# Performance work log

Hardware: AMD Instinct MI355X
Metric: run time of the kernel (lower is better)

## Reference

```python
import jax, jax.numpy as jnp
import numpy as np

B, S, C = 64, 1024, 512
EPS = 1e-5

def setup_inputs() -> dict:
    key = jax.random.key(0)
    k1, k2, k3 = jax.random.split(key, 3)
    x = jax.random.normal(k1, (B, S, C), dtype=jnp.float32)
    # LayerNorm affine over normalized_shape=[S, C]
    ln_w = jnp.ones((S, C), dtype=jnp.float32)
    ln_b = jnp.zeros((S, C), dtype=jnp.float32)
    # Linear(seq_len, seq_len): torch init U(-1/sqrt(S), 1/sqrt(S))
    bound = 1.0 / np.sqrt(S)
    lin_w = jax.random.uniform(k2, (S, S), jnp.float32, -bound, bound)
    lin_b = jax.random.uniform(k3, (S,), jnp.float32, -bound, bound)
    return {"x": x, "ln_w": ln_w, "ln_b": ln_b, "lin_w": lin_w, "lin_b": lin_b}

def reference(x, ln_w, ln_b, lin_w, lin_b):
    # LayerNorm over last two dims [S, C]
    mu = jnp.mean(x, axis=(1, 2), keepdims=True)
    var = jnp.mean(jnp.square(x - mu), axis=(1, 2), keepdims=True)
    h = (x - mu) * jax.lax.rsqrt(var + EPS) * ln_w + ln_b
    # permute -> [B, C, S], linear over S, relu, permute back, residual
    # fused as einsum over the seq axis directly (no explicit transpose)
    y = jnp.einsum('bsc,ts->btc', h, lin_w) + lin_b[None, :, None]
    y = jax.nn.relu(y)
    return x + y
```

## Files before the change

kernel.cpp:

```cpp
#include <hip/hip_runtime.h>
#include <stdint.h>

#define BB 64
#define SS 1024
#define CC 512
#define EPS 1e-5f

typedef __attribute__((ext_vector_type(8))) __bf16 bf16x8;
typedef __attribute__((ext_vector_type(8))) unsigned short ushort8v;
typedef __attribute__((ext_vector_type(4))) float f32x4;

__device__ __forceinline__ unsigned short f2bf(float f) {
    unsigned int u = __builtin_bit_cast(unsigned int, f);
    u += 0x7fffu + ((u >> 16) & 1u);
    return (unsigned short)(u >> 16);
}

__global__ __launch_bounds__(256) void k_prep(const float* __restrict__ x,
                                              const float* __restrict__ w,
                                              float* __restrict__ psum,
                                              float* __restrict__ psq,
                                              unsigned short* __restrict__ wb) {
    int t = threadIdx.x;
    if (blockIdx.x >= 2048) {
        int i = (blockIdx.x - 2048) * 256 + t;
        float4 v = ((const float4*)w)[i];
        ushort4 o;
        o.x = f2bf(v.x); o.y = f2bf(v.y); o.z = f2bf(v.z); o.w = f2bf(v.w);
        ((ushort4*)wb)[i] = o;
        return;
    }
    int b = blockIdx.x >> 5, g = blockIdx.x & 31;
    const float4* x4 = (const float4*)(x + (size_t)b * SS * CC + (size_t)g * 16384);
    float s = 0.f, q = 0.f;
#pragma unroll
    for (int i = 0; i < 16; ++i) {
        float4 v = x4[t + i * 256];
        s += v.x + v.y + v.z + v.w;
        q += v.x * v.x + v.y * v.y + v.z * v.z + v.w * v.w;
    }
    for (int off = 32; off; off >>= 1) {
        s += __shfl_down(s, off, 64);
        q += __shfl_down(q, off, 64);
    }
    __shared__ float ls[4], lq[4];
    int wv = t >> 6;
    if ((t & 63) == 0) { ls[wv] = s; lq[wv] = q; }
    __syncthreads();
    if (t == 0) {
        psum[blockIdx.x] = ls[0] + ls[1] + ls[2] + ls[3];
        psq[blockIdx.x]  = lq[0] + lq[1] + lq[2] + lq[3];
    }
}

__global__ __launch_bounds__(256) void k_norm_t(const float* __restrict__ x,
                                                const float* __restrict__ lnw,
                                                const float* __restrict__ lnb,
                                                const float* __restrict__ psum,
                                                const float* __restrict__ psq,
                                                unsigned short* __restrict__ Ht) {
    int idx = blockIdx.x;
    int b = idx >> 7;
    int rem = idx & 127;
    int s0 = (rem >> 3) << 6;
    int c0 = (rem & 7) << 6;
    int t = threadIdx.x;

    __shared__ float s_stats[2];
    if (t < 64) {
        float s = (t < 32) ? psum[b * 32 + t] : 0.f;
        float q = (t < 32) ? psq[b * 32 + t] : 0.f;
        for (int off = 16; off; off >>= 1) {
            s += __shfl_down(s, off, 64);
            q += __shfl_down(q, off, 64);
        }
        if (t == 0) {
            const float inv = 1.f / (float)(SS * CC);
            float m = s * inv;
            float v = q * inv - m * m;
            s_stats[0] = m;
            s_stats[1] = rsqrtf(v + EPS);
        }
    }
    __syncthreads();
    float mu = s_stats[0], rs = s_stats[1];

    __shared__ uint32_t lds[64 * 33];
    int cq = t & 15, spA = t >> 4;
#pragma unroll
    for (int h = 0; h < 2; ++h) {
        int sp = spA + h * 16;
        int sl = s0 + 2 * sp;
        int cc = c0 + 4 * cq;
        size_t xb = ((size_t)b * SS + sl) * CC + cc;
        size_t lb = (size_t)sl * CC + cc;
        float4 xv0 = *(const float4*)(x + xb);
        float4 xv1 = *(const float4*)(x + xb + CC);
        float4 wv0 = *(const float4*)(lnw + lb);
        float4 wv1 = *(const float4*)(lnw + lb + CC);
        float4 bv0 = *(const float4*)(lnb + lb);
        float4 bv1 = *(const float4*)(lnb + lb + CC);
        uint32_t u0 = (uint32_t)f2bf((xv0.x - mu) * rs * wv0.x + bv0.x) |
                      ((uint32_t)f2bf((xv1.x - mu) * rs * wv1.x + bv1.x) << 16);
        uint32_t u1 = (uint32_t)f2bf((xv0.y - mu) * rs * wv0.y + bv0.y) |
                      ((uint32_t)f2bf((xv1.y - mu) * rs * wv1.y + bv1.y) << 16);
        uint32_t u2 = (uint32_t)f2bf((xv0.z - mu) * rs * wv0.z + bv0.z) |
                      ((uint32_t)f2bf((xv1.z - mu) * rs * wv1.z + bv1.z) << 16);
        uint32_t u3 = (uint32_t)f2bf((xv0.w - mu) * rs * wv0.w + bv0.w) |
                      ((uint32_t)f2bf((xv1.w - mu) * rs * wv1.w + bv1.w) << 16);
        lds[(4 * cq + 0) * 33 + sp] = u0;
        lds[(4 * cq + 1) * 33 + sp] = u1;
        lds[(4 * cq + 2) * 33 + sp] = u2;
        lds[(4 * cq + 3) * 33 + sp] = u3;
    }
    __syncthreads();
    int spq = t & 7, clA = t >> 3;
#pragma unroll
    for (int h = 0; h < 2; ++h) {
        int cl = clA + h * 32;
        uint4 v;
        v.x = lds[cl * 33 + spq * 4 + 0];
        v.y = lds[cl * 33 + spq * 4 + 1];
        v.z = lds[cl * 33 + spq * 4 + 2];
        v.w = lds[cl * 33 + spq * 4 + 3];
        size_t o = (((size_t)b * CC + c0 + cl) * SS + (size_t)s0 + spq * 8) >> 3;
        ((uint4*)Ht)[o] = v;
    }
}

__global__ __launch_bounds__(256) void k_gemm(const unsigned short* __restrict__ A,
                                              const unsigned short* __restrict__ Bt,
                                              const float* __restrict__ x,
                                              const float* __restrict__ linb,
                                              float* __restrict__ out) {
    const int b = blockIdx.z;
    const int tm = blockIdx.y;
    const int tn = blockIdx.x;
    __shared__ __align__(16) unsigned short As[2][4096];
    __shared__ __align__(16) unsigned short Bs[2][4096];
    const int tid = threadIdx.x;
    const int lane = tid & 63;
    const int w = tid >> 6;
    const int wm = w >> 1, wn = w & 1;
    const int quad = lane >> 4, l15 = lane & 15;

    f32x4 acc[4][4];
#pragma unroll
    for (int mi = 0; mi < 4; ++mi)
#pragma unroll
        for (int ni = 0; ni < 4; ++ni)
            acc[mi][ni] = (f32x4){0.f, 0.f, 0.f, 0.f};

    const unsigned short* gA = A + ((size_t)(tm * 128 + w * 16 + l15)) * 1024 + quad * 8;
    const unsigned short* gB = Bt + ((size_t)b * 512 + tn * 128 + w * 16 + l15) * 1024 + quad * 8;

#pragma unroll
    for (int q = 0; q < 2; ++q) {
        __builtin_amdgcn_global_load_lds(
            (const __attribute__((address_space(1))) void*)(gA + q * 65536),
            (__attribute__((address_space(3))) void*)(As[0] + (q * 4 + w) * 512), 16, 0, 0);
        __builtin_amdgcn_global_load_lds(
            (const __attribute__((address_space(1))) void*)(gB + q * 65536),
            (__attribute__((address_space(3))) void*)(Bs[0] + (q * 4 + w) * 512), 16, 0, 0);
    }

    for (int it = 0; it < 32; ++it) {
        __syncthreads();
        if (it < 31) {
            const int k0 = (it + 1) * 32;
            const int nb = (it + 1) & 1;
#pragma unroll
            for (int q = 0; q < 2; ++q) {
                __builtin_amdgcn_global_load_lds(
                    (const __attribute__((address_space(1))) void*)(gA + q * 65536 + k0),
                    (__attribute__((address_space(3))) void*)(As[nb] + (q * 4 + w) * 512), 16, 0, 0);
                __builtin_amdgcn_global_load_lds(
                    (const __attribute__((address_space(1))) void*)(gB + q * 65536 + k0),
                    (__attribute__((address_space(3))) void*)(Bs[nb] + (q * 4 + w) * 512), 16, 0, 0);
            }
        }
        const int cb = it & 1;
        bf16x8 av[4], bv[4];
#pragma unroll
        for (int i = 0; i < 4; ++i) {
            ushort8v a = *(const ushort8v*)(As[cb] + (wm * 4 + i) * 512 + lane * 8);
            ushort8v bb = *(const ushort8v*)(Bs[cb] + (wn * 4 + i) * 512 + lane * 8);
            av[i] = __builtin_bit_cast(bf16x8, a);
            bv[i] = __builtin_bit_cast(bf16x8, bb);
        }
#pragma unroll
        for (int mi = 0; mi < 4; ++mi)
#pragma unroll
            for (int ni = 0; ni < 4; ++ni)
                acc[mi][ni] = __builtin_amdgcn_mfma_f32_16x16x32_bf16(
                    av[mi], bv[ni], acc[mi][ni], 0, 0, 0);
    }

#pragma unroll
    for (int mi = 0; mi < 4; ++mi) {
#pragma unroll
        for (int r = 0; r < 4; ++r) {
            int tt = tm * 128 + wm * 64 + mi * 16 + quad * 4 + r;
            float lb = linb[tt];
#pragma unroll
            for (int ni = 0; ni < 4; ++ni) {
                int cc = tn * 128 + wn * 64 + ni * 16 + l15;
                size_t o = ((size_t)b * SS + tt) * CC + cc;
                float v = acc[mi][ni][r] + lb;
                v = v > 0.f ? v : 0.f;
                out[o] = x[o] + v;
            }
        }
    }
}

extern "C" void kernel_launch(void* const* d_in, const int* in_sizes, int n_in,
                              void* d_out, int out_size, void* d_ws, size_t ws_size,
                              hipStream_t stream) {
    (void)in_sizes; (void)n_in; (void)out_size; (void)ws_size;
    const float* x    = (const float*)d_in[0];
    const float* lnw  = (const float*)d_in[1];
    const float* lnb  = (const float*)d_in[2];
    const float* linw = (const float*)d_in[3];
    const float* linb = (const float*)d_in[4];
    float* out = (float*)d_out;

    char* ws = (char*)d_ws;
    unsigned short* Wb = (unsigned short*)ws;
    unsigned short* Ht = (unsigned short*)(ws + (2u << 20));
    float* psum = (float*)(ws + (66u << 20));
    float* psq  = psum + 2048;

    k_prep<<<3072, 256, 0, stream>>>(x, linw, psum, psq, Wb);
    k_norm_t<<<8192, 256, 0, stream>>>(x, lnw, lnb, psum, psq, Ht);
    dim3 g(4, 8, 64);
    k_gemm<<<g, 256, 0, stream>>>(Wb, Ht, x, linb, out);
}
```

Baseline: 413.0 us.

## Drop GEMM double buffering for single-buffer K=64 steps; inline norm stats

The GEMM main loop moves from a double-buffered K=32 prefetch pipeline to a single LDS buffer holding K=64 per step, with a sync after the loads and two MFMA sub-steps per iteration. That halves the number of iterations and barriers, but global loads no longer overlap with MFMA compute inside a block, so it relies on other resident blocks to hide latency. The norm kernel also has every thread sum the 32 partial statistics itself, which removes a shuffle reduction and a block barrier at the cost of redundant loads.

```diff
diff --git a/kernel.cpp b/kernel.cpp
--- a/kernel.cpp
+++ b/kernel.cpp
@@ -66,24 +66,15 @@
     int c0 = (rem & 7) << 6;
     int t = threadIdx.x;
 
-    __shared__ float s_stats[2];
-    if (t < 64) {
-        float s = (t < 32) ? psum[b * 32 + t] : 0.f;
-        float q = (t < 32) ? psq[b * 32 + t] : 0.f;
-        for (int off = 16; off; off >>= 1) {
-            s += __shfl_down(s, off, 64);
-            q += __shfl_down(q, off, 64);
-        }
-        if (t == 0) {
-            const float inv = 1.f / (float)(SS * CC);
-            float m = s * inv;
-            float v = q * inv - m * m;
-            s_stats[0] = m;
-            s_stats[1] = rsqrtf(v + EPS);
-        }
-    }
-    __syncthreads();
-    float mu = s_stats[0], rs = s_stats[1];
+    float s = 0.f, q = 0.f;
+#pragma unroll
+    for (int i = 0; i < 32; ++i) {
+        s += psum[b * 32 + i];
+        q += psq[b * 32 + i];
+    }
+    const float inv = 1.f / (float)(SS * CC);
+    float mu = s * inv;
+    float rs = rsqrtf(q * inv - mu * mu + EPS);
 
     __shared__ uint32_t lds[64 * 33];
     int cq = t & 15, spA = t >> 4;
@@ -136,8 +127,8 @@
     const int b = blockIdx.z;
     const int tm = blockIdx.y;
     const int tn = blockIdx.x;
-    __shared__ __align__(16) unsigned short As[2][4096];
-    __shared__ __align__(16) unsigned short Bs[2][4096];
+    __shared__ __align__(16) unsigned short As[16 * 512];
+    __shared__ __align__(16) unsigned short Bs[16 * 512];
     const int tid = threadIdx.x;
     const int lane = tid & 63;
     const int w = tid >> 6;
@@ -151,49 +142,44 @@
         for (int ni = 0; ni < 4; ++ni)
             acc[mi][ni] = (f32x4){0.f, 0.f, 0.f, 0.f};
 
-    const unsigned short* gA = A + ((size_t)(tm * 128 + w * 16 + l15)) * 1024 + quad * 8;
-    const unsigned short* gB = Bt + ((size_t)b * 512 + tn * 128 + w * 16 + l15) * 1024 + quad * 8;
-
-#pragma unroll
-    for (int q = 0; q < 2; ++q) {
-        __builtin_amdgcn_global_load_lds(
-            (const __attribute__((address_space(1))) void*)(gA + q * 65536),
-            (__attribute__((address_space(3))) void*)(As[0] + (q * 4 + w) * 512), 16, 0, 0);
-        __builtin_amdgcn_global_load_lds(
-            (const __attribute__((address_space(1))) void*)(gB + q * 65536),
-            (__attribute__((address_space(3))) void*)(Bs[0] + (q * 4 + w) * 512), 16, 0, 0);
-    }
-
-    for (int it = 0; it < 32; ++it) {
+    const unsigned short* gA = A + ((size_t)(tm * 128 + w * 32 + l15)) * 1024 + quad * 8;
+    const unsigned short* gB = Bt + ((size_t)b * 512 + tn * 128 + w * 32 + l15) * 1024 + quad * 8;
+
+    for (int it = 0; it < 16; ++it) {
+        const int k0 = it * 64;
         __syncthreads();
-        if (it < 31) {
-            const int k0 = (it + 1) * 32;
-            const int nb = (it + 1) & 1;
-#pragma unroll
-            for (int q = 0; q < 2; ++q) {
+#pragma unroll
+        for (int j = 0; j < 2; ++j) {
+#pragma unroll
+            for (int kk = 0; kk < 2; ++kk) {
                 __builtin_amdgcn_global_load_lds(
-                    (const __attribute__((address_space(1))) void*)(gA + q * 65536 + k0),
-                    (__attribute__((address_space(3))) void*)(As[nb] + (q * 4 + w) * 512), 16, 0, 0);
+                    (const __attribute__((address_space(1))) void*)(gA + j * 16384 + k0 + kk * 32),
+                    (__attribute__((address_space(3))) void*)(As + ((2 * w + j) * 2 + kk) * 512),
+                    16, 0, 0);
                 __builtin_amdgcn_global_load_lds(
-                    (const __attribute__((address_space(1))) void*)(gB + q * 65536 + k0),
-                    (__attribute__((address_space(3))) void*)(Bs[nb] + (q * 4 + w) * 512), 16, 0, 0);
+                    (const __attribute__((address_space(1))) void*)(gB + j * 16384 + k0 + kk * 32),
+                    (__attribute__((address_space(3))) void*)(Bs + ((2 * w + j) * 2 + kk) * 512),
+                    16, 0, 0);
             }
         }
-        const int cb = it & 1;
-        bf16x8 av[4], bv[4];
-#pragma unroll
-        for (int i = 0; i < 4; ++i) {
-            ushort8v a = *(const ushort8v*)(As[cb] + (wm * 4 + i) * 512 + lane * 8);
-            ushort8v bb = *(const ushort8v*)(Bs[cb] + (wn * 4 + i) * 512 + lane * 8);
-            av[i] = __builtin_bit_cast(bf16x8, a);
-            bv[i] = __builtin_bit_cast(bf16x8, bb);
+        __syncthreads();
+#pragma unroll
+        for (int kk = 0; kk < 2; ++kk) {
+            bf16x8 av[4], bv[4];
+#pragma unroll
+            for (int i = 0; i < 4; ++i) {
+                ushort8v a = *(const ushort8v*)(As + ((wm * 4 + i) * 2 + kk) * 512 + lane * 8);
+                ushort8v bb = *(const ushort8v*)(Bs + ((wn * 4 + i) * 2 + kk) * 512 + lane * 8);
+                av[i] = __builtin_bit_cast(bf16x8, a);
+                bv[i] = __builtin_bit_cast(bf16x8, bb);
+            }
+#pragma unroll
+            for (int mi = 0; mi < 4; ++mi)
+#pragma unroll
+                for (int ni = 0; ni < 4; ++ni)
+                    acc[mi][ni] = __builtin_amdgcn_mfma_f32_16x16x32_bf16(
+                        av[mi], bv[ni], acc[mi][ni], 0, 0, 0);
         }
-#pragma unroll
-        for (int mi = 0; mi < 4; ++mi)
-#pragma unroll
-            for (int ni = 0; ni < 4; ++ni)
-                acc[mi][ni] = __builtin_amdgcn_mfma_f32_16x16x32_bf16(
-                    av[mi], bv[ni], acc[mi][ni], 0, 0, 0);
     }
 
 #pragma unroll
```

After: 404.3 us. 2.1% less time.
